# Performance work log

Hardware: AMD Instinct MI355X
Metric: run time of the kernel (lower is better)

## Reference

```python
import jax, jax.numpy as jnp
import numpy as np

N_NODES = 8192
N_EDGES = 65536
D_MODEL = 64
D_INNER = 128
D_STATE = 16
DT_RANK = 4
LAYER_NUM = 3
TAU = 0.01


def _unif(key, shape, fan_out):
    stdv = 1.0 / np.sqrt(fan_out)
    return jax.random.uniform(key, shape, jnp.float32, -stdv, stdv)


def setup_inputs() -> dict:
    key = jax.random.key(0)
    ks = jax.random.split(key, 12)
    x = jax.random.normal(ks[0], (N_NODES, D_MODEL), jnp.float32)
    edge_index = jax.random.randint(ks[1], (2, N_EDGES), 0, N_NODES, jnp.int64)
    in_proj_w = _unif(ks[2], (D_MODEL, 2 * D_INNER), 2 * D_INNER)
    x_proj_w = _unif(ks[3], (D_INNER, DT_RANK + 2 * D_STATE), DT_RANK + 2 * D_STATE)
    dt_proj_w = _unif(ks[4], (DT_RANK, D_INNER), D_INNER)
    out_proj_w = _unif(ks[5], (D_INNER, D_MODEL), D_MODEL)
    A_log = jnp.log(jnp.broadcast_to(jnp.arange(1, D_STATE + 1, dtype=jnp.float32)[None, :], (D_INNER, D_STATE)))
    D = jnp.ones((D_INNER,), jnp.float32)
    in_act_w = _unif(ks[6], (D_INNER, 2), 2)
    in_act_b = _unif(ks[7], (2,), 2)
    out_act_w = _unif(ks[8], (D_INNER, 2), 2)
    out_act_b = _unif(ks[9], (2,), 2)
    return {"x": x, "in_proj_w": in_proj_w, "x_proj_w": x_proj_w, "dt_proj_w": dt_proj_w,
            "A_log": A_log, "D": D, "out_proj_w": out_proj_w,
            "in_act_w": in_act_w, "in_act_b": in_act_b, "out_act_w": out_act_w, "out_act_b": out_act_b,
            "edge_index": edge_index, "layer_num": LAYER_NUM}


def _norm_adj(row, col, w, n_nodes):
    # SparseTensor(...).set_diag() adds diag value 1; symmetric deg^-1/2 renorm
    deg = jax.ops.segment_sum(w, row, num_segments=n_nodes) + 1.0
    dinv = jnp.where(deg > 0, deg ** -0.5, 0.0)
    return dinv[row] * w * dinv[col], dinv * dinv  # off-diag edge weights, diag weights


def _spmm(row, col, ew, dw, x, n_nodes):
    # adj @ x with adj = edges(ew) + diag(dw); x: [N, F]
    return jax.ops.segment_sum(ew[:, None] * x[col], row, num_segments=n_nodes) + dw[:, None] * x


def _gumbel_hard(logits, key, tau):
    g = jax.random.gumbel(key, logits.shape, logits.dtype)
    y = jax.nn.softmax((logits + g) / tau, axis=-1)
    hard = jax.nn.one_hot(jnp.argmax(y, axis=-1), logits.shape[-1], dtype=y.dtype)
    return hard + y - jax.lax.stop_gradient(y)


def reference(x, in_proj_w, x_proj_w, dt_proj_w, A_log, D, out_proj_w,
              in_act_w, in_act_b, out_act_w, out_act_b, edge_index, layer_num):
    n_nodes, d_model = x.shape
    d_inner = dt_proj_w.shape[1]
    n = A_log.shape[1]
    dt_rank = dt_proj_w.shape[0]
    row, col = edge_index[0], edge_index[1]

    xl = jnp.broadcast_to(x[:, None, :], (n_nodes, layer_num, d_model))  # [N,L,d_model]
    x_and_res = xl @ in_proj_w                                           # [N,L,2*d_inner]
    xs, res = jnp.split(x_and_res, 2, axis=-1)
    xs = jax.nn.relu(xs)                                                 # u in scan

    A = -jnp.exp(A_log)                                                  # [d_inner, n]
    x_dbl = xs @ x_proj_w                                                # [N,L,dt_rank+2n]
    delta = jax.nn.softplus(x_dbl[..., :dt_rank] @ dt_proj_w)            # [N,L,d_inner]
    B = x_dbl[..., dt_rank:dt_rank + n]                                  # [N,L,n]
    C = x_dbl[..., dt_rank + n:]                                         # [N,L,n]

    deltaA = jnp.exp(jnp.einsum('bld,dn->bldn', delta, A))               # [N,L,d_inner,n]
    deltaB_u = jnp.einsum('bld,bln->bldn', delta * xs, B)                # [N,L,d_inner,n]

    # initial adjacency: unit-weight edges, sym-normalized with self loops
    ew, dw = _norm_adj(row, col, jnp.ones((row.shape[0],), xs.dtype), n_nodes)
    state = jnp.zeros((n_nodes, d_inner, n), xs.dtype)
    gkey = jax.random.key(42)
    ys = []
    for i in range(layer_num):  # small fixed number of GCN/SSM steps
        state = deltaA[:, i] * state + deltaB_u[:, i]
        y = jnp.einsum('bdn,bn->bd', state, C[:, i])                     # [N,d_inner]
        flat = _spmm(row, col, ew, dw, state.reshape(n_nodes, d_inner * n), n_nodes)
        state = flat.reshape(n_nodes, d_inner, n)
        in_p = _gumbel_hard(y @ in_act_w + in_act_b, jax.random.fold_in(gkey, 2 * i), TAU)
        out_p = _gumbel_hard(y @ out_act_w + out_act_b, jax.random.fold_in(gkey, 2 * i + 1), TAU)
        w = in_p[col, 0] * out_p[row, 0]  # keep_in_prob[v] * keep_out_prob[u]
        ew, dw = _norm_adj(row, col, w, n_nodes)
        ys.append(y)

    y = jnp.stack(ys, axis=1) + xs * D                                   # [N,L,d_inner]
    y = y * jax.nn.relu(res)
    out = y @ out_proj_w                                                 # [N,L,d_model]
    return out[:, -1, :]
```

## Files before the change

kernel.cpp:

```cpp
#include <hip/hip_runtime.h>
#include <cstdint>

#define NN 8192
#define NE 65536
#define G 8
#define CAP 64

typedef _Float16 h8 __attribute__((ext_vector_type(8)));
typedef _Float16 h2 __attribute__((ext_vector_type(2)));

__host__ __device__ inline void tf2x32(uint32_t k0, uint32_t k1,
                                       uint32_t x0, uint32_t x1,
                                       uint32_t& r0, uint32_t& r1) {
  uint32_t ks2 = k0 ^ k1 ^ 0x1BD11BDAu;
  x0 += k0; x1 += k1;
#define TF_ROT(x,d) (((x)<<(d))|((x)>>(32-(d))))
#define TF_R4(ra,rb,rc,rd) \
  x0+=x1; x1=TF_ROT(x1,ra); x1^=x0; \
  x0+=x1; x1=TF_ROT(x1,rb); x1^=x0; \
  x0+=x1; x1=TF_ROT(x1,rc); x1^=x0; \
  x0+=x1; x1=TF_ROT(x1,rd); x1^=x0;
  TF_R4(13,15,26,6)  x0+=k1;  x1+=ks2+1u;
  TF_R4(17,29,16,24) x0+=ks2; x1+=k0+2u;
  TF_R4(13,15,26,6)  x0+=k0;  x1+=k1+3u;
  TF_R4(17,29,16,24) x0+=k1;  x1+=ks2+4u;
  TF_R4(13,15,26,6)  x0+=ks2; x1+=k0+5u;
  r0=x0; r1=x1;
#undef TF_R4
#undef TF_ROT
}

__device__ inline float gumbel32(uint32_t k0, uint32_t k1, uint32_t idx) {
  uint32_t a, b;
  tf2x32(k0, k1, 0u, idx, a, b);
  uint32_t bits = a ^ b;
  float f = __uint_as_float((bits >> 9) | 0x3f800000u) - 1.0f;
  float u = (f > 0.0f) ? f : 1.17549435e-38f;
  return -logf(-logf(u));
}

__global__ __launch_bounds__(256) void k_nodeprep(
    const float* __restrict__ x, const float* __restrict__ ipw,
    const float* __restrict__ xpw, const float* __restrict__ dtw,
    const float* __restrict__ iaw, const float* __restrict__ iab,
    const float* __restrict__ oaw, const float* __restrict__ oab,
    const float* __restrict__ alog, const float* __restrict__ wout,
    const int* __restrict__ ei,
    uint32_t ki0, uint32_t ki1, uint32_t ko0, uint32_t ko1,
    float* __restrict__ xs, float* __restrict__ rres,
    float* __restrict__ delta, _Float16* __restrict__ dxh2,
    float* __restrict__ Bm, _Float16* __restrict__ Bh,
    float* __restrict__ Cm,
    float* __restrict__ inp, float* __restrict__ outp,
    float* __restrict__ Amat, _Float16* __restrict__ woT,
    int* __restrict__ cnt, int* __restrict__ csr_col) {
  __shared__ float sx[G][64];
  __shared__ float sxs[G][128];
  __shared__ float sdbl[G][36];
  __shared__ float sdx[G][128];
  int t = threadIdx.x;
  int b0 = blockIdx.x * G;
  if (t < 64) {
    int e = blockIdx.x * 64 + t;
    int v = ei[e];
    int pos = atomicAdd(&cnt[v], 1);
    if (pos < CAP) csr_col[(v<<6) + pos] = ei[NE + e];
  }
  {
    int i = blockIdx.x * 8 + (t & 7);
    if (t < 8) {
      int d = i >> 6, oc = i & 63;
      woT[oc*128 + d] = (_Float16)wout[i];
    }
  }
  if (blockIdx.x == 0) {
    for (int i = t; i < 2048; i += 256) Amat[i] = -expf(alog[i]);
  }
  for (int i = t; i < G*64; i += 256) sx[i>>6][i&63] = x[b0*64 + i];
  __syncthreads();
  float acc[G];
#pragma unroll
  for (int g = 0; g < G; g++) acc[g] = 0.f;
  for (int k = 0; k < 64; k++) {
    float w = ipw[k*256 + t];
#pragma unroll
    for (int g = 0; g < G; g++) acc[g] += sx[g][k] * w;
  }
  if (t < 128) {
#pragma unroll
    for (int g = 0; g < G; g++) {
      float v = fmaxf(acc[g], 0.f);
      sxs[g][t] = v;
      xs[(size_t)(b0+g)*128 + t] = v;
    }
  } else {
    int j = t - 128;
#pragma unroll
    for (int g = 0; g < G; g++) rres[(size_t)(b0+g)*128 + j] = fmaxf(acc[g], 0.f);
  }
  __syncthreads();
  for (int idx = t; idx < G*36; idx += 256) {
    int g = idx / 36, c = idx % 36;
    float a = 0.f;
    for (int d = 0; d < 128; d++) a += sxs[g][d] * xpw[d*36 + c];
    sdbl[g][c] = a;
    if (c >= 4 && c < 20) {
      Bm[(b0+g)*16 + (c-4)] = a;
      Bh[(b0+g)*16 + (c-4)] = (_Float16)a;
    } else if (c >= 20)    Cm[(b0+g)*16 + (c-20)] = a;
  }
  __syncthreads();
  {
    int d = t & 127, hi = t >> 7;
#pragma unroll
    for (int gg = 0; gg < G/2; gg++) {
      int g = hi*(G/2) + gg;
      int b = b0 + g;
      float dt = sdbl[g][0]*dtw[d]     + sdbl[g][1]*dtw[128+d]
               + sdbl[g][2]*dtw[256+d] + sdbl[g][3]*dtw[384+d];
      float dv = fmaxf(dt, 0.f) + log1pf(expf(-fabsf(dt)));
      delta[(size_t)b*128 + d] = dv;
      sdx[g][d] = dv * sxs[g][d];
    }
  }
  __syncthreads();
  for (int i = t; i < G*64; i += 256) {
    int g = i >> 6, d = i & 63;
    h2 pk;
    pk.x = (_Float16)sdx[g][d];
    pk.y = (_Float16)sdx[g][d + 64];
    ((h2*)(dxh2 + ((size_t)(b0+g) << 7)))[d] = pk;
  }
  int wid = t >> 6, lane = t & 63;
#pragma unroll
  for (int s = 0; s < 2; s++) {
    int g = wid*2 + s;
    int b = b0 + g;
    float da = sdx[g][lane], db = sdx[g][lane + 64];
    float4 pr;
    pr.x = da*iaw[2*lane]   + db*iaw[2*(lane+64)];
    pr.y = da*iaw[2*lane+1] + db*iaw[2*(lane+64)+1];
    pr.z = da*oaw[2*lane]   + db*oaw[2*(lane+64)];
    pr.w = da*oaw[2*lane+1] + db*oaw[2*(lane+64)+1];
    for (int off = 32; off >= 1; off >>= 1) {
      pr.x += __shfl_down(pr.x, off);
      pr.y += __shfl_down(pr.y, off);
      pr.z += __shfl_down(pr.z, off);
      pr.w += __shfl_down(pr.w, off);
    }
    float gsel = 0.f;
    if (lane < 4) {
      uint32_t kk0 = (lane < 2) ? ki0 : ko0;
      uint32_t kk1 = (lane < 2) ? ki1 : ko1;
      gsel = gumbel32(kk0, kk1, 2u*(uint32_t)b + (uint32_t)(lane & 1));
    }
    float g0 = __shfl(gsel, 0), g1 = __shfl(gsel, 1);
    float g2 = __shfl(gsel, 2), g3 = __shfl(gsel, 3);
    if (lane == 0) {
      float BC = 0.f;
      for (int n = 0; n < 16; n++) BC += sdbl[g][4+n] * sdbl[g][20+n];
      float li0 = BC*pr.x + iab[0], li1 = BC*pr.y + iab[1];
      float lo0 = BC*pr.z + oab[0], lo1 = BC*pr.w + oab[1];
      inp[b]  = (li0 + g0 >= li1 + g1) ? 1.0f : 0.0f;
      outp[b] = (lo0 + g2 >= lo1 + g3) ? 1.0f : 0.0f;
    }
  }
}

__global__ __launch_bounds__(256) void k_spmm0f(
    const int* __restrict__ cnt, const int* __restrict__ csr_col,
    const float* __restrict__ inp, const float* __restrict__ outp,
    const float* __restrict__ delta, const _Float16* __restrict__ dxh2,
    const float* __restrict__ Bm, const _Float16* __restrict__ Bh,
    const float* __restrict__ Cm, const float* __restrict__ Amat,
    _Float16* __restrict__ s_out, float* __restrict__ dinv1,
    float* __restrict__ y2p) {
  __shared__ int   sc[CAP];
  __shared__ float scoef[CAP];
  __shared__ float sdeg;
  int t = threadIdx.x;
  int v = blockIdx.x;
  int deg = min(cnt[v], CAP);
  if (t < 64) {
    float g = 0.f;
    if (t < deg) {
      int c = csr_col[(v<<6) + t];
      sc[t] = c;
      scoef[t] = 1.0f / sqrtf((float)min(cnt[c], CAP) + 1.0f);
      g = inp[c];
    }
    for (int off = 32; off >= 1; off >>= 1) g += __shfl_down(g, off);
    if (t == 0) sdeg = g;
  }
  __syncthreads();
  int js = t & 1, nq = (t >> 1) & 1, d0 = t >> 2, d1 = d0 + 64;
  float dv = 1.0f / sqrtf((float)deg + 1.0f);
  const float4* BmV = (const float4*)(Bm + ((size_t)v << 4));
  float4 Bv0 = BmV[nq*2], Bv1 = BmV[nq*2+1];
  h2 pkv = ((const h2*)(dxh2 + ((size_t)v << 7)))[d0];
  float dx0 = (float)pkv.x, dx1 = (float)pkv.y;
  float4 a0l = {0.f,0.f,0.f,0.f}, a0h = {0.f,0.f,0.f,0.f};
  float4 a1l = {0.f,0.f,0.f,0.f}, a1h = {0.f,0.f,0.f,0.f};
#pragma unroll 2
  for (int j = js; j < deg; j += 2) {
    int c = sc[j];
    float coef = dv * scoef[j];
    h2 pk = ((const h2*)(dxh2 + ((size_t)c << 7)))[d0];
    h8 Bp = ((const h8*)(Bh + ((size_t)c << 4)))[nq];
    float e0 = coef * (float)pk.x;
    float e1 = coef * (float)pk.y;
    float b0f = (float)Bp[0], b1f = (float)Bp[1], b2f = (float)Bp[2], b3f = (float)Bp[3];
    float b4f = (float)Bp[4], b5f = (float)Bp[5], b6f = (float)Bp[6], b7f = (float)Bp[7];
    a0l.x += e0*b0f; a0l.y += e0*b1f; a0l.z += e0*b2f; a0l.w += e0*b3f;
    a0h.x += e0*b4f; a0h.y += e0*b5f; a0h.z += e0*b6f; a0h.w += e0*b7f;
    a1l.x += e1*b0f; a1l.y += e1*b1f; a1l.z += e1*b2f; a1l.w += e1*b3f;
    a1h.x += e1*b4f; a1h.y += e1*b5f; a1h.z += e1*b6f; a1h.w += e1*b7f;
  }
  a0l.x += __shfl_xor(a0l.x, 1); a0l.y += __shfl_xor(a0l.y, 1);
  a0l.z += __shfl_xor(a0l.z, 1); a0l.w += __shfl_xor(a0l.w, 1);
  a0h.x += __shfl_xor(a0h.x, 1); a0h.y += __shfl_xor(a0h.y, 1);
  a0h.z += __shfl_xor(a0h.z, 1); a0h.w += __shfl_xor(a0h.w, 1);
  a1l.x += __shfl_xor(a1l.x, 1); a1l.y += __shfl_xor(a1l.y, 1);
  a1l.z += __shfl_xor(a1l.z, 1); a1l.w += __shfl_xor(a1l.w, 1);
  a1h.x += __shfl_xor(a1h.x, 1); a1h.y += __shfl_xor(a1h.y, 1);
  a1h.z += __shfl_xor(a1h.z, 1); a1h.w += __shfl_xor(a1h.w, 1);
  float dw = dv * dv;
  float c0 = dw * dx0, c1 = dw * dx1;
  a0l.x += c0*Bv0.x; a0l.y += c0*Bv0.y; a0l.z += c0*Bv0.z; a0l.w += c0*Bv0.w;
  a0h.x += c0*Bv1.x; a0h.y += c0*Bv1.y; a0h.z += c0*Bv1.z; a0h.w += c0*Bv1.w;
  a1l.x += c1*Bv0.x; a1l.y += c1*Bv0.y; a1l.z += c1*Bv0.z; a1l.w += c1*Bv0.w;
  a1h.x += c1*Bv1.x; a1h.y += c1*Bv1.y; a1h.z += c1*Bv1.z; a1h.w += c1*Bv1.w;
  float de0 = delta[v*128 + d0], de1 = delta[v*128 + d1];
  const float4* A0p = (const float4*)(Amat + (d0 << 4));
  const float4* A1p = (const float4*)(Amat + (d1 << 4));
  float4 A00 = A0p[nq*2], A01 = A0p[nq*2+1];
  float4 A10 = A1p[nq*2], A11 = A1p[nq*2+1];
  float4 E0l, E0h, E1l, E1h;
  E0l.x = expf(de0*A00.x); E0l.y = expf(de0*A00.y); E0l.z = expf(de0*A00.z); E0l.w = expf(de0*A00.w);
  E0h.x = expf(de0*A01.x); E0h.y = expf(de0*A01.y); E0h.z = expf(de0*A01.z); E0h.w = expf(de0*A01.w);
  E1l.x = expf(de1*A10.x); E1l.y = expf(de1*A10.y); E1l.z = expf(de1*A10.z); E1l.w = expf(de1*A10.w);
  E1h.x = expf(de1*A11.x); E1h.y = expf(de1*A11.y); E1h.z = expf(de1*A11.z); E1h.w = expf(de1*A11.w);
  float4 s0l, s0h, s1l, s1h;
  s0l.x = E0l.x*a0l.x + dx0*Bv0.x; s0l.y = E0l.y*a0l.y + dx0*Bv0.y;
  s0l.z = E0l.z*a0l.z + dx0*Bv0.z; s0l.w = E0l.w*a0l.w + dx0*Bv0.w;
  s0h.x = E0h.x*a0h.x + dx0*Bv1.x; s0h.y = E0h.y*a0h.y + dx0*Bv1.y;
  s0h.z = E0h.z*a0h.z + dx0*Bv1.z; s0h.w = E0h.w*a0h.w + dx0*Bv1.w;
  s1l.x = E1l.x*a1l.x + dx1*Bv0.x; s1l.y = E1l.y*a1l.y + dx1*Bv0.y;
  s1l.z = E1l.z*a1l.z + dx1*Bv0.z; s1l.w = E1l.w*a1l.w + dx1*Bv0.w;
  s1h.x = E1h.x*a1h.x + dx1*Bv1.x; s1h.y = E1h.y*a1h.y + dx1*Bv1.y;
  s1h.z = E1h.z*a1h.z + dx1*Bv1.z; s1h.w = E1h.w*a1h.w + dx1*Bv1.w;
  if (inp[v] != 0.f && js == 0) {
    h8* op = (h8*)(s_out + ((size_t)v << 11));
    h8 p0, p1;
    p0[0]=(_Float16)s0l.x; p0[1]=(_Float16)s0l.y; p0[2]=(_Float16)s0l.z; p0[3]=(_Float16)s0l.w;
    p0[4]=(_Float16)s0h.x; p0[5]=(_Float16)s0h.y; p0[6]=(_Float16)s0h.z; p0[7]=(_Float16)s0h.w;
    p1[0]=(_Float16)s1l.x; p1[1]=(_Float16)s1l.y; p1[2]=(_Float16)s1l.z; p1[3]=(_Float16)s1l.w;
    p1[4]=(_Float16)s1h.x; p1[5]=(_Float16)s1h.y; p1[6]=(_Float16)s1h.z; p1[7]=(_Float16)s1h.w;
    op[d0*2 + nq] = p0;
    op[d0*2 + 128 + nq] = p1;
  }
  float degs = sdeg;
  float d1v = 1.0f / sqrtf(outp[v]*degs + 1.0f);
  if (t == 0) dinv1[v] = d1v;
  float dw1 = d1v * d1v;
  const float4* CmV = (const float4*)(Cm + ((size_t)v << 4));
  float4 Cv0 = CmV[nq*2], Cv1 = CmV[nq*2+1];
  float BvC = Bv0.x*Cv0.x + Bv0.y*Cv0.y + Bv0.z*Cv0.z + Bv0.w*Cv0.w
            + Bv1.x*Cv1.x + Bv1.y*Cv1.y + Bv1.z*Cv1.z + Bv1.w*Cv1.w;
  float y0p = dw1*(E0l.x*s0l.x*Cv0.x + E0l.y*s0l.y*Cv0.y + E0l.z*s0l.z*Cv0.z + E0l.w*s0l.w*Cv0.w
                 + E0h.x*s0h.x*Cv1.x + E0h.y*s0h.y*Cv1.y + E0h.z*s0h.z*Cv1.z + E0h.w*s0h.w*Cv1.w)
            + dx0*BvC;
  float y1p = dw1*(E1l.x*s1l.x*Cv0.x + E1l.y*s1l.y*Cv0.y + E1l.z*s1l.z*Cv0.z + E1l.w*s1l.w*Cv0.w
                 + E1h.x*s1h.x*Cv1.x + E1h.y*s1h.y*Cv1.y + E1h.z*s1h.z*Cv1.z + E1h.w*s1h.w*Cv1.w)
            + dx1*BvC;
  y0p += __shfl_xor(y0p, 2);
  y1p += __shfl_xor(y1p, 2);
  if ((t & 3) == 0) {
    y2p[v*128 + d0] = y0p;
    y2p[v*128 + d1] = y1p;
  }
}

__global__ __launch_bounds__(256) void k_spmm1fo(
    const int* __restrict__ cnt, const int* __restrict__ csr_col,
    const float* __restrict__ dinv1,
    const float* __restrict__ inp, const float* __restrict__ outp,
    const float* __restrict__ delta,
    const float* __restrict__ Cm, const float* __restrict__ Amat,
    const _Float16* __restrict__ s_in, const float* __restrict__ y2p,
    const float* __restrict__ xs, const float* __restrict__ rres,
    const float* __restrict__ Dv, const _Float16* __restrict__ woT,
    float* __restrict__ out) {
  __shared__ int   sc[CAP];
  __shared__ float scoef[CAP];
  __shared__ int   snact;
  __shared__ float ty[128];
  __shared__ float sproj[3][64];
  __shared__ h8 swoT[1024];
  int t = threadIdx.x;
  int v = blockIdx.x;
  {
    const uint4* src = (const uint4*)woT;
    uint4* dst = (uint4*)swoT;
    for (int i = t; i < 1024; i += 256) {
      int oc = i >> 4, c = i & 15;
      dst[(oc << 4) | (c ^ (oc & 7))] = src[i];
    }
  }
  if (t == 0) snact = 0;
  if (t < 64) {
    int deg = (outp[v] != 0.f) ? min(cnt[v], CAP) : 0;
    if (t < deg) {
      int c = csr_col[(v<<6) + t];
      if (inp[c] != 0.f) {
        int p = atomicAdd(&snact, 1);
        sc[p] = c; scoef[p] = dinv1[c];
      }
    }
  }
  __syncthreads();
  int nact = snact;
  int js = t & 1, nq = (t >> 1) & 1, d0 = t >> 2, d1 = d0 + 64;
  float dv = dinv1[v];
  float4 a0l = {0.f,0.f,0.f,0.f}, a0h = {0.f,0.f,0.f,0.f};
  float4 a1l = {0.f,0.f,0.f,0.f}, a1h = {0.f,0.f,0.f,0.f};
#pragma unroll 2
  for (int j = js; j < nact; j += 2) {
    int c = sc[j];
    float coef = dv * scoef[j];
    const h8* rp = (const h8*)(s_in + ((size_t)c << 11));
    h8 n0 = rp[d0*2 + nq], n1 = rp[d0*2 + 128 + nq];
    a0l.x += coef*(float)n0[0]; a0l.y += coef*(float)n0[1];
    a0l.z += coef*(float)n0[2]; a0l.w += coef*(float)n0[3];
    a0h.x += coef*(float)n0[4]; a0h.y += coef*(float)n0[5];
    a0h.z += coef*(float)n0[6]; a0h.w += coef*(float)n0[7];
    a1l.x += coef*(float)n1[0]; a1l.y += coef*(float)n1[1];
    a1l.z += coef*(float)n1[2]; a1l.w += coef*(float)n1[3];
    a1h.x += coef*(float)n1[4]; a1h.y += coef*(float)n1[5];
    a1h.z += coef*(float)n1[6]; a1h.w += coef*(float)n1[7];
  }
  a0l.x += __shfl_xor(a0l.x, 1); a0l.y += __shfl_xor(a0l.y, 1);
  a0l.z += __shfl_xor(a0l.z, 1); a0l.w += __shfl_xor(a0l.w, 1);
  a0h.x += __shfl_xor(a0h.x, 1); a0h.y += __shfl_xor(a0h.y, 1);
  a0h.z += __shfl_xor(a0h.z, 1); a0h.w += __shfl_xor(a0h.w, 1);
  a1l.x += __shfl_xor(a1l.x, 1); a1l.y += __shfl_xor(a1l.y, 1);
  a1l.z += __shfl_xor(a1l.z, 1); a1l.w += __shfl_xor(a1l.w, 1);
  a1h.x += __shfl_xor(a1h.x, 1); a1h.y += __shfl_xor(a1h.y, 1);
  a1h.z += __shfl_xor(a1h.z, 1); a1h.w += __shfl_xor(a1h.w, 1);
  float y0g = 0.f, y1g = 0.f;
  if (nact > 0) {
    float de0 = delta[v*128 + d0], de1 = delta[v*128 + d1];
    const float4* A0p = (const float4*)(Amat + (d0 << 4));
    const float4* A1p = (const float4*)(Amat + (d1 << 4));
    float4 A00 = A0p[nq*2], A01 = A0p[nq*2+1];
    float4 A10 = A1p[nq*2], A11 = A1p[nq*2+1];
    const float4* CmV = (const float4*)(Cm + ((size_t)v << 4));
    float4 Cv0 = CmV[nq*2], Cv1 = CmV[nq*2+1];
    y0g = expf(de0*A00.x)*a0l.x*Cv0.x + expf(de0*A00.y)*a0l.y*Cv0.y
        + expf(de0*A00.z)*a0l.z*Cv0.z + expf(de0*A00.w)*a0l.w*Cv0.w
        + expf(de0*A01.x)*a0h.x*Cv1.x + expf(de0*A01.y)*a0h.y*Cv1.y
        + expf(de0*A01.z)*a0h.z*Cv1.z + expf(de0*A01.w)*a0h.w*Cv1.w;
    y1g = expf(de1*A10.x)*a1l.x*Cv0.x + expf(de1*A10.y)*a1l.y*Cv0.y
        + expf(de1*A10.z)*a1l.z*Cv0.z + expf(de1*A10.w)*a1l.w*Cv0.w
        + expf(de1*A11.x)*a1h.x*Cv1.x + expf(de1*A11.y)*a1h.y*Cv1.y
        + expf(de1*A11.z)*a1h.z*Cv1.z + expf(de1*A11.w)*a1h.w*Cv1.w;
  }
  y0g += __shfl_xor(y0g, 2);
  y1g += __shfl_xor(y1g, 2);
  if ((t & 3) == 0) {
    float yA = y0g + y2p[v*128 + d0];
    float yB = y1g + y2p[v*128 + d1];
    ty[d0] = (yA + xs[v*128 + d0]*Dv[d0]) * rres[v*128 + d0];
    ty[d1] = (yB + xs[v*128 + d1]*Dv[d1]) * rres[v*128 + d1];
  }
  __syncthreads();
  int oc = t & 63, ks = t >> 6;
  const float4* tyv = (const float4*)ty;
  float acc = 0.f;
#pragma unroll
  for (int i = 0; i < 4; i++) {
    int c = (ks << 2) + i;
    h8 wv = swoT[(oc << 4) | (c ^ (oc & 7))];
    float4 t0 = tyv[c*2], t1 = tyv[c*2+1];
    acc += t0.x*(float)wv[0] + t0.y*(float)wv[1] + t0.z*(float)wv[2] + t0.w*(float)wv[3]
         + t1.x*(float)wv[4] + t1.y*(float)wv[5] + t1.z*(float)wv[6] + t1.w*(float)wv[7];
  }
  if (ks > 0) sproj[ks-1][oc] = acc;
  __syncthreads();
  if (ks == 0) out[v*64 + oc] = acc + sproj[0][oc] + sproj[1][oc] + sproj[2][oc];
}

extern "C" void kernel_launch(void* const* d_in, const int* in_sizes, int n_in,
                              void* d_out, int out_size, void* d_ws, size_t ws_size,
                              hipStream_t stream) {
  const float* x    = (const float*)d_in[0];
  const float* ipw  = (const float*)d_in[1];
  const float* xpw  = (const float*)d_in[2];
  const float* dtw  = (const float*)d_in[3];
  const float* alog = (const float*)d_in[4];
  const float* Dv   = (const float*)d_in[5];
  const float* wout = (const float*)d_in[6];
  const float* iaw  = (const float*)d_in[7];
  const float* iab  = (const float*)d_in[8];
  const float* oaw  = (const float*)d_in[9];
  const float* oab  = (const float*)d_in[10];
  const int*   ei   = (const int*)d_in[11];
  (void)in_sizes; (void)n_in; (void)out_size; (void)ws_size;

  float* W = (float*)d_ws;
  size_t o = 0;
  float* xs    = W + o; o += (size_t)NN*128;
  float* rres  = W + o; o += (size_t)NN*128;
  float* delta = W + o; o += (size_t)NN*128;
  float* y2p   = W + o; o += (size_t)NN*128;
  float* Bm    = W + o; o += (size_t)NN*16;
  float* Cm    = W + o; o += (size_t)NN*16;
  float* Amat  = W + o; o += 2048;
  float* dinv1 = W + o; o += NN;
  float* inp   = W + o; o += NN;
  float* outp  = W + o; o += NN;
  _Float16* dxh2 = (_Float16*)(W + o); o += (size_t)NN*64;
  _Float16* Bh   = (_Float16*)(W + o); o += (size_t)NN*8;
  _Float16* woT  = (_Float16*)(W + o); o += 4096;
  _Float16* stA  = (_Float16*)(W + o); o += (size_t)NN*1024;
  int* cnt     = (int*)(W + o);
  int* csr_col = cnt + NN;

  uint32_t ki0, ki1, ko0, ko1;
  tf2x32(0u, 42u, 0u, 0u, ki0, ki1);
  tf2x32(0u, 42u, 0u, 1u, ko0, ko1);

  hipMemsetAsync(cnt, 0, NN*sizeof(int), stream);

  k_nodeprep<<<NN/G, 256, 0, stream>>>(x, ipw, xpw, dtw, iaw, iab, oaw, oab,
                                       alog, wout, ei, ki0, ki1, ko0, ko1,
                                       xs, rres, delta, dxh2, Bm, Bh, Cm,
                                       inp, outp, Amat, woT, cnt, csr_col);

  k_spmm0f<<<NN, 256, 0, stream>>>(cnt, csr_col, inp, outp,
                                   delta, dxh2, Bm, Bh, Cm, Amat,
                                   stA, dinv1, y2p);

  k_spmm1fo<<<NN, 256, 0, stream>>>(cnt, csr_col, dinv1, inp, outp,
                                    delta, Cm, Amat, stA, y2p,
                                    xs, rres, Dv, woT, (float*)d_out);
}
```

Before: 171.4 us.

## Map one wavefront per node in SpMM kernels and drop fp16 B copy

Both SpMM kernels now handle four nodes per block, one 64-lane wavefront per node, with each lane owning a channel pair and all 16 states. This removes the block-wide __syncthreads, the cross-lane shuffle reductions, and the shared-memory staging of the transposed output weights. The first kernel reads fp32 B rows directly instead of a half-precision copy. The second kernel skips inactive neighbours in place instead of compacting them with shared atomics. The node-prep matmuls are also vectorised with float4 shared loads. In exchange, each lane holds far more registers (32 accumulators plus B values), which may lower occupancy, and it does 2x more neighbour-gather work serially per lane.

```diff
diff --git a/kernel.cpp b/kernel.cpp
--- a/kernel.cpp
+++ b/kernel.cpp
@@ -49,8 +49,7 @@
     uint32_t ki0, uint32_t ki1, uint32_t ko0, uint32_t ko1,
     float* __restrict__ xs, float* __restrict__ rres,
     float* __restrict__ delta, _Float16* __restrict__ dxh2,
-    float* __restrict__ Bm, _Float16* __restrict__ Bh,
-    float* __restrict__ Cm,
+    float* __restrict__ Bm, float* __restrict__ Cm,
     float* __restrict__ inp, float* __restrict__ outp,
     float* __restrict__ Amat, _Float16* __restrict__ woT,
     int* __restrict__ cnt, int* __restrict__ csr_col) {
@@ -81,10 +80,16 @@
   float acc[G];
 #pragma unroll
   for (int g = 0; g < G; g++) acc[g] = 0.f;
-  for (int k = 0; k < 64; k++) {
-    float w = ipw[k*256 + t];
-#pragma unroll
-    for (int g = 0; g < G; g++) acc[g] += sx[g][k] * w;
+  for (int k4 = 0; k4 < 16; k4++) {
+    float w0 = ipw[(k4*4+0)*256 + t];
+    float w1 = ipw[(k4*4+1)*256 + t];
+    float w2 = ipw[(k4*4+2)*256 + t];
+    float w3 = ipw[(k4*4+3)*256 + t];
+#pragma unroll
+    for (int g = 0; g < G; g++) {
+      float4 xv = ((const float4*)&sx[g][0])[k4];
+      acc[g] += xv.x*w0; acc[g] += xv.y*w1; acc[g] += xv.z*w2; acc[g] += xv.w*w3;
+    }
   }
   if (t < 128) {
 #pragma unroll
@@ -102,12 +107,16 @@
   for (int idx = t; idx < G*36; idx += 256) {
     int g = idx / 36, c = idx % 36;
     float a = 0.f;
-    for (int d = 0; d < 128; d++) a += sxs[g][d] * xpw[d*36 + c];
+    for (int d4 = 0; d4 < 32; d4++) {
+      float4 sv = ((const float4*)&sxs[g][0])[d4];
+      a += sv.x*xpw[(d4*4+0)*36 + c];
+      a += sv.y*xpw[(d4*4+1)*36 + c];
+      a += sv.z*xpw[(d4*4+2)*36 + c];
+      a += sv.w*xpw[(d4*4+3)*36 + c];
+    }
     sdbl[g][c] = a;
-    if (c >= 4 && c < 20) {
-      Bm[(b0+g)*16 + (c-4)] = a;
-      Bh[(b0+g)*16 + (c-4)] = (_Float16)a;
-    } else if (c >= 20)    Cm[(b0+g)*16 + (c-20)] = a;
+    if (c >= 4 && c < 20)  Bm[(b0+g)*16 + (c-4)]  = a;
+    else if (c >= 20)      Cm[(b0+g)*16 + (c-20)] = a;
   }
   __syncthreads();
   {
@@ -171,114 +180,110 @@
     const int* __restrict__ cnt, const int* __restrict__ csr_col,
     const float* __restrict__ inp, const float* __restrict__ outp,
     const float* __restrict__ delta, const _Float16* __restrict__ dxh2,
-    const float* __restrict__ Bm, const _Float16* __restrict__ Bh,
-    const float* __restrict__ Cm, const float* __restrict__ Amat,
+    const float* __restrict__ Bm, const float* __restrict__ Cm,
+    const float* __restrict__ Amat,
     _Float16* __restrict__ s_out, float* __restrict__ dinv1,
     float* __restrict__ y2p) {
-  __shared__ int   sc[CAP];
-  __shared__ float scoef[CAP];
-  __shared__ float sdeg;
-  int t = threadIdx.x;
-  int v = blockIdx.x;
+  __shared__ int   sc[4][CAP];
+  __shared__ float scf[4][CAP];
+  int t = threadIdx.x, wid = t >> 6, lane = t & 63;
+  int v = (blockIdx.x << 2) + wid;
   int deg = min(cnt[v], CAP);
-  if (t < 64) {
-    float g = 0.f;
-    if (t < deg) {
-      int c = csr_col[(v<<6) + t];
-      sc[t] = c;
-      scoef[t] = 1.0f / sqrtf((float)min(cnt[c], CAP) + 1.0f);
-      g = inp[c];
-    }
-    for (int off = 32; off >= 1; off >>= 1) g += __shfl_down(g, off);
-    if (t == 0) sdeg = g;
-  }
-  __syncthreads();
-  int js = t & 1, nq = (t >> 1) & 1, d0 = t >> 2, d1 = d0 + 64;
+  float gl = 0.f;
+  if (lane < deg) {
+    int c = csr_col[(v << 6) + lane];
+    sc[wid][lane] = c;
+    scf[wid][lane] = 1.0f / sqrtf((float)min(cnt[c], CAP) + 1.0f);
+    gl = inp[c];
+  }
+  float degs = gl;
+#pragma unroll
+  for (int off = 32; off >= 1; off >>= 1) degs += __shfl_xor(degs, off);
+  asm volatile("s_waitcnt lgkmcnt(0)" ::: "memory");
+  int d0 = lane, d1 = lane + 64;
   float dv = 1.0f / sqrtf((float)deg + 1.0f);
-  const float4* BmV = (const float4*)(Bm + ((size_t)v << 4));
-  float4 Bv0 = BmV[nq*2], Bv1 = BmV[nq*2+1];
   h2 pkv = ((const h2*)(dxh2 + ((size_t)v << 7)))[d0];
   float dx0 = (float)pkv.x, dx1 = (float)pkv.y;
-  float4 a0l = {0.f,0.f,0.f,0.f}, a0h = {0.f,0.f,0.f,0.f};
-  float4 a1l = {0.f,0.f,0.f,0.f}, a1h = {0.f,0.f,0.f,0.f};
+  float Bf[16];
+  {
+    const float4* p = (const float4*)(Bm + ((size_t)v << 4));
+    float4 q0 = p[0], q1 = p[1], q2 = p[2], q3 = p[3];
+    Bf[0]=q0.x; Bf[1]=q0.y; Bf[2]=q0.z; Bf[3]=q0.w;
+    Bf[4]=q1.x; Bf[5]=q1.y; Bf[6]=q1.z; Bf[7]=q1.w;
+    Bf[8]=q2.x; Bf[9]=q2.y; Bf[10]=q2.z; Bf[11]=q2.w;
+    Bf[12]=q3.x; Bf[13]=q3.y; Bf[14]=q3.z; Bf[15]=q3.w;
+  }
+  float a0[16], a1[16];
+  {
+    float dw = dv * dv;
+    float c0 = dw * dx0, c1 = dw * dx1;
+#pragma unroll
+    for (int n = 0; n < 16; n++) { a0[n] = c0*Bf[n]; a1[n] = c1*Bf[n]; }
+  }
 #pragma unroll 2
-  for (int j = js; j < deg; j += 2) {
-    int c = sc[j];
-    float coef = dv * scoef[j];
+  for (int j = 0; j < deg; j++) {
+    int c = sc[wid][j];
+    float coef = dv * scf[wid][j];
     h2 pk = ((const h2*)(dxh2 + ((size_t)c << 7)))[d0];
-    h8 Bp = ((const h8*)(Bh + ((size_t)c << 4)))[nq];
+    const float4* bp = (const float4*)(Bm + ((size_t)c << 4));
+    float4 B0 = bp[0], B1 = bp[1], B2 = bp[2], B3 = bp[3];
     float e0 = coef * (float)pk.x;
     float e1 = coef * (float)pk.y;
-    float b0f = (float)Bp[0], b1f = (float)Bp[1], b2f = (float)Bp[2], b3f = (float)Bp[3];
-    float b4f = (float)Bp[4], b5f = (float)Bp[5], b6f = (float)Bp[6], b7f = (float)Bp[7];
-    a0l.x += e0*b0f; a0l.y += e0*b1f; a0l.z += e0*b2f; a0l.w += e0*b3f;
-    a0h.x += e0*b4f; a0h.y += e0*b5f; a0h.z += e0*b6f; a0h.w += e0*b7f;
-    a1l.x += e1*b0f; a1l.y += e1*b1f; a1l.z += e1*b2f; a1l.w += e1*b3f;
-    a1h.x += e1*b4f; a1h.y += e1*b5f; a1h.z += e1*b6f; a1h.w += e1*b7f;
-  }
-  a0l.x += __shfl_xor(a0l.x, 1); a0l.y += __shfl_xor(a0l.y, 1);
-  a0l.z += __shfl_xor(a0l.z, 1); a0l.w += __shfl_xor(a0l.w, 1);
-  a0h.x += __shfl_xor(a0h.x, 1); a0h.y += __shfl_xor(a0h.y, 1);
-  a0h.z += __shfl_xor(a0h.z, 1); a0h.w += __shfl_xor(a0h.w, 1);
-  a1l.x += __shfl_xor(a1l.x, 1); a1l.y += __shfl_xor(a1l.y, 1);
-  a1l.z += __shfl_xor(a1l.z, 1); a1l.w += __shfl_xor(a1l.w, 1);
-  a1h.x += __shfl_xor(a1h.x, 1); a1h.y += __shfl_xor(a1h.y, 1);
-  a1h.z += __shfl_xor(a1h.z, 1); a1h.w += __shfl_xor(a1h.w, 1);
-  float dw = dv * dv;
-  float c0 = dw * dx0, c1 = dw * dx1;
-  a0l.x += c0*Bv0.x; a0l.y += c0*Bv0.y; a0l.z += c0*Bv0.z; a0l.w += c0*Bv0.w;
-  a0h.x += c0*Bv1.x; a0h.y += c0*Bv1.y; a0h.z += c0*Bv1.z; a0h.w += c0*Bv1.w;
-  a1l.x += c1*Bv0.x; a1l.y += c1*Bv0.y; a1l.z += c1*Bv0.z; a1l.w += c1*Bv0.w;
-  a1h.x += c1*Bv1.x; a1h.y += c1*Bv1.y; a1h.z += c1*Bv1.z; a1h.w += c1*Bv1.w;
-  float de0 = delta[v*128 + d0], de1 = delta[v*128 + d1];
+    a0[0]+=e0*B0.x; a0[1]+=e0*B0.y; a0[2]+=e0*B0.z; a0[3]+=e0*B0.w;
+    a0[4]+=e0*B1.x; a0[5]+=e0*B1.y; a0[6]+=e0*B1.z; a0[7]+=e0*B1.w;
+    a0[8]+=e0*B2.x; a0[9]+=e0*B2.y; a0[10]+=e0*B2.z; a0[11]+=e0*B2.w;
+    a0[12]+=e0*B3.x; a0[13]+=e0*B3.y; a0[14]+=e0*B3.z; a0[15]+=e0*B3.w;
+    a1[0]+=e1*B0.x; a1[1]+=e1*B0.y; a1[2]+=e1*B0.z; a1[3]+=e1*B0.w;
+    a1[4]+=e1*B1.x; a1[5]+=e1*B1.y; a1[6]+=e1*B1.z; a1[7]+=e1*B1.w;
+    a1[8]+=e1*B2.x; a1[9]+=e1*B2.y; a1[10]+=e1*B2.z; a1[11]+=e1*B2.w;
+    a1[12]+=e1*B3.x; a1[13]+=e1*B3.y; a1[14]+=e1*B3.z; a1[15]+=e1*B3.w;
+  }
+  float de0 = delta[(size_t)v*128 + d0], de1 = delta[(size_t)v*128 + d1];
   const float4* A0p = (const float4*)(Amat + (d0 << 4));
   const float4* A1p = (const float4*)(Amat + (d1 << 4));
-  float4 A00 = A0p[nq*2], A01 = A0p[nq*2+1];
-  float4 A10 = A1p[nq*2], A11 = A1p[nq*2+1];
-  float4 E0l, E0h, E1l, E1h;
-  E0l.x = expf(de0*A00.x); E0l.y = expf(de0*A00.y); E0l.z = expf(de0*A00.z); E0l.w = expf(de0*A00.w);
-  E0h.x = expf(de0*A01.x); E0h.y = expf(de0*A01.y); E0h.z = expf(de0*A01.z); E0h.w = expf(de0*A01.w);
-  E1l.x = expf(de1*A10.x); E1l.y = expf(de1*A10.y); E1l.z = expf(de1*A10.z); E1l.w = expf(de1*A10.w);
-  E1h.x = expf(de1*A11.x); E1h.y = expf(de1*A11.y); E1h.z = expf(de1*A11.z); E1h.w = expf(de1*A11.w);
-  float4 s0l, s0h, s1l, s1h;
-  s0l.x = E0l.x*a0l.x + dx0*Bv0.x; s0l.y = E0l.y*a0l.y + dx0*Bv0.y;
-  s0l.z = E0l.z*a0l.z + dx0*Bv0.z; s0l.w = E0l.w*a0l.w + dx0*Bv0.w;
-  s0h.x = E0h.x*a0h.x + dx0*Bv1.x; s0h.y = E0h.y*a0h.y + dx0*Bv1.y;
-  s0h.z = E0h.z*a0h.z + dx0*Bv1.z; s0h.w = E0h.w*a0h.w + dx0*Bv1.w;
-  s1l.x = E1l.x*a1l.x + dx1*Bv0.x; s1l.y = E1l.y*a1l.y + dx1*Bv0.y;
-  s1l.z = E1l.z*a1l.z + dx1*Bv0.z; s1l.w = E1l.w*a1l.w + dx1*Bv0.w;
-  s1h.x = E1h.x*a1h.x + dx1*Bv1.x; s1h.y = E1h.y*a1h.y + dx1*Bv1.y;
-  s1h.z = E1h.z*a1h.z + dx1*Bv1.z; s1h.w = E1h.w*a1h.w + dx1*Bv1.w;
-  if (inp[v] != 0.f && js == 0) {
+  const float4* Cp  = (const float4*)(Cm + ((size_t)v << 4));
+  float d1v = 1.0f / sqrtf(outp[v]*degs + 1.0f);
+  if (lane == 0) dinv1[v] = d1v;
+  float dw1 = d1v * d1v;
+  float y0 = 0.f, y1 = 0.f, BvC = 0.f;
+  _Float16 sh0[16], sh1[16];
+#pragma unroll
+  for (int q = 0; q < 4; q++) {
+    float4 Aq0 = A0p[q], Aq1 = A1p[q], Cq = Cp[q];
+    float A0a[4] = {Aq0.x, Aq0.y, Aq0.z, Aq0.w};
+    float A1a[4] = {Aq1.x, Aq1.y, Aq1.z, Aq1.w};
+    float Ca[4]  = {Cq.x, Cq.y, Cq.z, Cq.w};
+#pragma unroll
+    for (int i = 0; i < 4; i++) {
+      int n = 4*q + i;
+      float E0 = expf(de0 * A0a[i]);
+      float E1 = expf(de1 * A1a[i]);
+      float s0 = E0*a0[n] + dx0*Bf[n];
+      float s1 = E1*a1[n] + dx1*Bf[n];
+      y0 += E0*s0*Ca[i];
+      y1 += E1*s1*Ca[i];
+      BvC += Bf[n]*Ca[i];
+      sh0[n] = (_Float16)s0;
+      sh1[n] = (_Float16)s1;
+    }
+  }
+  y0 = dw1*y0 + dx0*BvC;
+  y1 = dw1*y1 + dx1*BvC;
+  if (inp[v] != 0.f) {
+    h8 P00, P01, P10, P11;
+#pragma unroll
+    for (int i = 0; i < 8; i++) {
+      P00[i] = sh0[i]; P01[i] = sh0[8+i];
+      P10[i] = sh1[i]; P11[i] = sh1[8+i];
+    }
     h8* op = (h8*)(s_out + ((size_t)v << 11));
-    h8 p0, p1;
-    p0[0]=(_Float16)s0l.x; p0[1]=(_Float16)s0l.y; p0[2]=(_Float16)s0l.z; p0[3]=(_Float16)s0l.w;
-    p0[4]=(_Float16)s0h.x; p0[5]=(_Float16)s0h.y; p0[6]=(_Float16)s0h.z; p0[7]=(_Float16)s0h.w;
-    p1[0]=(_Float16)s1l.x; p1[1]=(_Float16)s1l.y; p1[2]=(_Float16)s1l.z; p1[3]=(_Float16)s1l.w;
-    p1[4]=(_Float16)s1h.x; p1[5]=(_Float16)s1h.y; p1[6]=(_Float16)s1h.z; p1[7]=(_Float16)s1h.w;
-    op[d0*2 + nq] = p0;
-    op[d0*2 + 128 + nq] = p1;
-  }
-  float degs = sdeg;
-  float d1v = 1.0f / sqrtf(outp[v]*degs + 1.0f);
-  if (t == 0) dinv1[v] = d1v;
-  float dw1 = d1v * d1v;
-  const float4* CmV = (const float4*)(Cm + ((size_t)v << 4));
-  float4 Cv0 = CmV[nq*2], Cv1 = CmV[nq*2+1];
-  float BvC = Bv0.x*Cv0.x + Bv0.y*Cv0.y + Bv0.z*Cv0.z + Bv0.w*Cv0.w
-            + Bv1.x*Cv1.x + Bv1.y*Cv1.y + Bv1.z*Cv1.z + Bv1.w*Cv1.w;
-  float y0p = dw1*(E0l.x*s0l.x*Cv0.x + E0l.y*s0l.y*Cv0.y + E0l.z*s0l.z*Cv0.z + E0l.w*s0l.w*Cv0.w
-                 + E0h.x*s0h.x*Cv1.x + E0h.y*s0h.y*Cv1.y + E0h.z*s0h.z*Cv1.z + E0h.w*s0h.w*Cv1.w)
-            + dx0*BvC;
-  float y1p = dw1*(E1l.x*s1l.x*Cv0.x + E1l.y*s1l.y*Cv0.y + E1l.z*s1l.z*Cv0.z + E1l.w*s1l.w*Cv0.w
-                 + E1h.x*s1h.x*Cv1.x + E1h.y*s1h.y*Cv1.y + E1h.z*s1h.z*Cv1.z + E1h.w*s1h.w*Cv1.w)
-            + dx1*BvC;
-  y0p += __shfl_xor(y0p, 2);
-  y1p += __shfl_xor(y1p, 2);
-  if ((t & 3) == 0) {
-    y2p[v*128 + d0] = y0p;
-    y2p[v*128 + d1] = y1p;
-  }
+    op[2*lane]           = P00;
+    op[2*lane + 1]       = P01;
+    op[128 + 2*lane]     = P10;
+    op[128 + 2*lane + 1] = P11;
+  }
+  y2p[(size_t)v*128 + d0] = y0;
+  y2p[(size_t)v*128 + d1] = y1;
 }
 
 __global__ __launch_bounds__(256) void k_spmm1fo(
@@ -291,103 +296,90 @@
     const float* __restrict__ xs, const float* __restrict__ rres,
     const float* __restrict__ Dv, const _Float16* __restrict__ woT,
     float* __restrict__ out) {
-  __shared__ int   sc[CAP];
-  __shared__ float scoef[CAP];
-  __shared__ int   snact;
-  __shared__ float ty[128];
-  __shared__ float sproj[3][64];
-  __shared__ h8 swoT[1024];
-  int t = threadIdx.x;
-  int v = blockIdx.x;
-  {
-    const uint4* src = (const uint4*)woT;
-    uint4* dst = (uint4*)swoT;
-    for (int i = t; i < 1024; i += 256) {
-      int oc = i >> 4, c = i & 15;
-      dst[(oc << 4) | (c ^ (oc & 7))] = src[i];
-    }
-  }
-  if (t == 0) snact = 0;
-  if (t < 64) {
-    int deg = (outp[v] != 0.f) ? min(cnt[v], CAP) : 0;
-    if (t < deg) {
-      int c = csr_col[(v<<6) + t];
-      if (inp[c] != 0.f) {
-        int p = atomicAdd(&snact, 1);
-        sc[p] = c; scoef[p] = dinv1[c];
-      }
-    }
-  }
-  __syncthreads();
-  int nact = snact;
-  int js = t & 1, nq = (t >> 1) & 1, d0 = t >> 2, d1 = d0 + 64;
-  float dv = dinv1[v];
-  float4 a0l = {0.f,0.f,0.f,0.f}, a0h = {0.f,0.f,0.f,0.f};
-  float4 a1l = {0.f,0.f,0.f,0.f}, a1h = {0.f,0.f,0.f,0.f};
+  __shared__ int   sc[4][CAP];
+  __shared__ float scf[4][CAP];
+  __shared__ float ty[4][128];
+  int t = threadIdx.x, wid = t >> 6, lane = t & 63;
+  int v = (blockIdx.x << 2) + wid;
+  int deg = (outp[v] != 0.f) ? min(cnt[v], CAP) : 0;
+  float gl = 0.f;
+  if (lane < deg) {
+    int c = csr_col[(v << 6) + lane];
+    float g = inp[c];
+    sc[wid][lane] = c;
+    scf[wid][lane] = (g != 0.f) ? dinv1[c] : 0.f;
+    gl = g;
+  }
+  unsigned long long mask = __ballot(lane < deg && gl != 0.f);
+  asm volatile("s_waitcnt lgkmcnt(0)" ::: "memory");
+  int d0 = lane, d1 = lane + 64;
+  float y0 = 0.f, y1 = 0.f;
+  if (mask != 0ull) {
+    float dv = dinv1[v];
+    float a0[16], a1[16];
+#pragma unroll
+    for (int n = 0; n < 16; n++) { a0[n] = 0.f; a1[n] = 0.f; }
 #pragma unroll 2
-  for (int j = js; j < nact; j += 2) {
-    int c = sc[j];
-    float coef = dv * scoef[j];
-    const h8* rp = (const h8*)(s_in + ((size_t)c << 11));
-    h8 n0 = rp[d0*2 + nq], n1 = rp[d0*2 + 128 + nq];
-    a0l.x += coef*(float)n0[0]; a0l.y += coef*(float)n0[1];
-    a0l.z += coef*(float)n0[2]; a0l.w += coef*(float)n0[3];
-    a0h.x += coef*(float)n0[4]; a0h.y += coef*(float)n0[5];
-    a0h.z += coef*(float)n0[6]; a0h.w += coef*(float)n0[7];
-    a1l.x += coef*(float)n1[0]; a1l.y += coef*(float)n1[1];
-    a1l.z += coef*(float)n1[2]; a1l.w += coef*(float)n1[3];
-    a1h.x += coef*(float)n1[4]; a1h.y += coef*(float)n1[5];
-    a1h.z += coef*(float)n1[6]; a1h.w += coef*(float)n1[7];
-  }
-  a0l.x += __shfl_xor(a0l.x, 1); a0l.y += __shfl_xor(a0l.y, 1);
-  a0l.z += __shfl_xor(a0l.z, 1); a0l.w += __shfl_xor(a0l.w, 1);
-  a0h.x += __shfl_xor(a0h.x, 1); a0h.y += __shfl_xor(a0h.y, 1);
-  a0h.z += __shfl_xor(a0h.z, 1); a0h.w += __shfl_xor(a0h.w, 1);
-  a1l.x += __shfl_xor(a1l.x, 1); a1l.y += __shfl_xor(a1l.y, 1);
-  a1l.z += __shfl_xor(a1l.z, 1); a1l.w += __shfl_xor(a1l.w, 1);
-  a1h.x += __shfl_xor(a1h.x, 1); a1h.y += __shfl_xor(a1h.y, 1);
-  a1h.z += __shfl_xor(a1h.z, 1); a1h.w += __shfl_xor(a1h.w, 1);
-  float y0g = 0.f, y1g = 0.f;
-  if (nact > 0) {
-    float de0 = delta[v*128 + d0], de1 = delta[v*128 + d1];
+    for (int j = 0; j < deg; j++) {
+      float cf = scf[wid][j];
+      if (cf == 0.f) continue;
+      int c = sc[wid][j];
+      float coef = dv * cf;
+      const h8* rp = (const h8*)(s_in + ((size_t)c << 11));
+      h8 n00 = rp[2*lane], n01 = rp[2*lane+1];
+      h8 n10 = rp[128 + 2*lane], n11 = rp[128 + 2*lane+1];
+      a0[0]+=coef*(float)n00[0]; a0[1]+=coef*(float)n00[1];
+      a0[2]+=coef*(float)n00[2]; a0[3]+=coef*(float)n00[3];
+      a0[4]+=coef*(float)n00[4]; a0[5]+=coef*(float)n00[5];
+      a0[6]+=coef*(float)n00[6]; a0[7]+=coef*(float)n00[7];
+      a0[8]+=coef*(float)n01[0]; a0[9]+=coef*(float)n01[1];
+      a0[10]+=coef*(float)n01[2]; a0[11]+=coef*(float)n01[3];
+      a0[12]+=coef*(float)n01[4]; a0[13]+=coef*(float)n01[5];
+      a0[14]+=coef*(float)n01[6]; a0[15]+=coef*(float)n01[7];
+      a1[0]+=coef*(float)n10[0]; a1[1]+=coef*(float)n10[1];
+      a1[2]+=coef*(float)n10[2]; a1[3]+=coef*(float)n10[3];
+      a1[4]+=coef*(float)n10[4]; a1[5]+=coef*(float)n10[5];
+      a1[6]+=coef*(float)n10[6]; a1[7]+=coef*(float)n10[7];
+      a1[8]+=coef*(float)n11[0]; a1[9]+=coef*(float)n11[1];
+      a1[10]+=coef*(float)n11[2]; a1[11]+=coef*(float)n11[3];
+      a1[12]+=coef*(float)n11[4]; a1[13]+=coef*(float)n11[5];
+      a1[14]+=coef*(float)n11[6]; a1[15]+=coef*(float)n11[7];
+    }
+    float de0 = delta[(size_t)v*128 + d0], de1 = delta[(size_t)v*128 + d1];
     const float4* A0p = (const float4*)(Amat + (d0 << 4));
     const float4* A1p = (const float4*)(Amat + (d1 << 4));
-    float4 A00 = A0p[nq*2], A01 = A0p[nq*2+1];
-    float4 A10 = A1p[nq*2], A11 = A1p[nq*2+1];
-    const float4* CmV = (const float4*)(Cm + ((size_t)v << 4));
-    float4 Cv0 = CmV[nq*2], Cv1 = CmV[nq*2+1];
-    y0g = expf(de0*A00.x)*a0l.x*Cv0.x + expf(de0*A00.y)*a0l.y*Cv0.y
-        + expf(de0*A00.z)*a0l.z*Cv0.z + expf(de0*A00.w)*a0l.w*Cv0.w
-        + expf(de0*A01.x)*a0h.x*Cv1.x + expf(de0*A01.y)*a0h.y*Cv1.y
-        + expf(de0*A01.z)*a0h.z*Cv1.z + expf(de0*A01.w)*a0h.w*Cv1.w;
-    y1g = expf(de1*A10.x)*a1l.x*Cv0.x + expf(de1*A10.y)*a1l.y*Cv0.y
-        + expf(de1*A10.z)*a1l.z*Cv0.z + expf(de1*A10.w)*a1l.w*Cv0.w
-        + expf(de1*A11.x)*a1h.x*Cv1.x + expf(de1*A11.y)*a1h.y*Cv1.y
-        + expf(de1*A11.z)*a1h.z*Cv1.z + expf(de1*A11.w)*a1h.w*Cv1.w;
-  }
-  y0g += __shfl_xor(y0g, 2);
-  y1g += __shfl_xor(y1g, 2);
-  if ((t & 3) == 0) {
-    float yA = y0g + y2p[v*128 + d0];
-    float yB = y1g + y2p[v*128 + d1];
-    ty[d0] = (yA + xs[v*128 + d0]*Dv[d0]) * rres[v*128 + d0];
-    ty[d1] = (yB + xs[v*128 + d1]*Dv[d1]) * rres[v*128 + d1];
-  }
-  __syncthreads();
-  int oc = t & 63, ks = t >> 6;
-  const float4* tyv = (const float4*)ty;
+    const float4* Cp  = (const float4*)(Cm + ((size_t)v << 4));
+#pragma unroll
+    for (int q = 0; q < 4; q++) {
+      float4 Aq0 = A0p[q], Aq1 = A1p[q], Cq = Cp[q];
+      float A0a[4] = {Aq0.x, Aq0.y, Aq0.z, Aq0.w};
+      float A1a[4] = {Aq1.x, Aq1.y, Aq1.z, Aq1.w};
+      float Ca[4]  = {Cq.x, Cq.y, Cq.z, Cq.w};
+#pragma unroll
+      for (int i = 0; i < 4; i++) {
+        int n = 4*q + i;
+        y0 += expf(de0*A0a[i]) * a0[n] * Ca[i];
+        y1 += expf(de1*A1a[i]) * a1[n] * Ca[i];
+      }
+    }
+  }
+  float t0 = (y0 + y2p[(size_t)v*128 + d0] + xs[(size_t)v*128 + d0]*Dv[d0]) * rres[(size_t)v*128 + d0];
+  float t1 = (y1 + y2p[(size_t)v*128 + d1] + xs[(size_t)v*128 + d1]*Dv[d1]) * rres[(size_t)v*128 + d1];
+  ty[wid][d0] = t0;
+  ty[wid][d1] = t1;
+  asm volatile("s_waitcnt lgkmcnt(0)" ::: "memory");
+  __builtin_amdgcn_sched_barrier(0);
   float acc = 0.f;
-#pragma unroll
-  for (int i = 0; i < 4; i++) {
-    int c = (ks << 2) + i;
-    h8 wv = swoT[(oc << 4) | (c ^ (oc & 7))];
-    float4 t0 = tyv[c*2], t1 = tyv[c*2+1];
-    acc += t0.x*(float)wv[0] + t0.y*(float)wv[1] + t0.z*(float)wv[2] + t0.w*(float)wv[3]
-         + t1.x*(float)wv[4] + t1.y*(float)wv[5] + t1.z*(float)wv[6] + t1.w*(float)wv[7];
-  }
-  if (ks > 0) sproj[ks-1][oc] = acc;
-  __syncthreads();
-  if (ks == 0) out[v*64 + oc] = acc + sproj[0][oc] + sproj[1][oc] + sproj[2][oc];
+  const float4* tyv = (const float4*)&ty[wid][0];
+  const h8* wrow = (const h8*)(woT + ((size_t)lane << 7));
+#pragma unroll
+  for (int ch = 0; ch < 16; ch++) {
+    h8 wv = wrow[ch];
+    float4 u0 = tyv[2*ch], u1 = tyv[2*ch+1];
+    acc += u0.x*(float)wv[0] + u0.y*(float)wv[1] + u0.z*(float)wv[2] + u0.w*(float)wv[3]
+         + u1.x*(float)wv[4] + u1.y*(float)wv[5] + u1.z*(float)wv[6] + u1.w*(float)wv[7];
+  }
+  out[(size_t)v*64 + lane] = acc;
 }
 
 extern "C" void kernel_launch(void* const* d_in, const int* in_sizes, int n_in,
@@ -420,7 +412,7 @@
   float* inp   = W + o; o += NN;
   float* outp  = W + o; o += NN;
   _Float16* dxh2 = (_Float16*)(W + o); o += (size_t)NN*64;
-  _Float16* Bh   = (_Float16*)(W + o); o += (size_t)NN*8;
+  o += (size_t)NN*8;
   _Float16* woT  = (_Float16*)(W + o); o += 4096;
   _Float16* stA  = (_Float16*)(W + o); o += (size_t)NN*1024;
   int* cnt     = (int*)(W + o);
@@ -434,14 +426,14 @@
 
   k_nodeprep<<<NN/G, 256, 0, stream>>>(x, ipw, xpw, dtw, iaw, iab, oaw, oab,
                                        alog, wout, ei, ki0, ki1, ko0, ko1,
-                                       xs, rres, delta, dxh2, Bm, Bh, Cm,
+                                       xs, rres, delta, dxh2, Bm, Cm,
                                        inp, outp, Amat, woT, cnt, csr_col);
 
-  k_spmm0f<<<NN, 256, 0, stream>>>(cnt, csr_col, inp, outp,
-                                   delta, dxh2, Bm, Bh, Cm, Amat,
-                                   stA, dinv1, y2p);
-
-  k_spmm1fo<<<NN, 256, 0, stream>>>(cnt, csr_col, dinv1, inp, outp,
-                                    delta, Cm, Amat, stA, y2p,
-                                    xs, rres, Dv, woT, (float*)d_out);
-}
+  k_spmm0f<<<NN/4, 256, 0, stream>>>(cnt, csr_col, inp, outp,
+                                     delta, dxh2, Bm, Cm, Amat,
+                                     stA, dinv1, y2p);
+
+  k_spmm1fo<<<NN/4, 256, 0, stream>>>(cnt, csr_col, dinv1, inp, outp,
+                                      delta, Cm, Amat, stA, y2p,
+                                      xs, rres, Dv, woT, (float*)d_out);
+}
```

Measured after the change: 160.2 us. 6.5% less time.
